# Kernel tuning notes

Measured on AMD Instinct MI355X. Metric: run time of the kernel, lower is better.

## Reference

```python
import jax, jax.numpy as jnp
import numpy as np

B, C, D, H, W = 1, 128, 8, 32, 32
NH, HD = 8, 16            # num_heads, head_dim = C // NH
PD, PH, PW = 2, 4, 4      # local patch dims
RD, RH, RW = 2, 2, 2      # global K/V reduction ratios
MLPH = 4 * C              # mlp_ratio = 4
EPS = 1e-5
SCALE = HD ** -0.5


def setup_inputs() -> dict:
    key = jax.random.key(0)
    ks = iter(jax.random.split(key, 16))
    def w(shape, scale=0.02):
        return jax.random.normal(next(ks), shape, jnp.float32) * scale
    inp = {"x": jax.random.normal(next(ks), (B, C, D, H, W), jnp.float32)}
    for p in ("l", "g"):  # local branch / global branch transformer blocks
        inp[f"{p}_n1_g"] = jnp.ones((C,), jnp.float32)
        inp[f"{p}_n1_b"] = jnp.zeros((C,), jnp.float32)
        inp[f"{p}_qkv_w"] = w((3 * C, C))            # Linear(dim, 3*dim, bias=False)
        inp[f"{p}_proj_w"] = w((C, C))
        inp[f"{p}_proj_b"] = jnp.zeros((C,), jnp.float32)
        inp[f"{p}_n2_g"] = jnp.ones((C,), jnp.float32)
        inp[f"{p}_n2_b"] = jnp.zeros((C,), jnp.float32)
        inp[f"{p}_fc1_w"] = w((MLPH, C))
        inp[f"{p}_fc1_b"] = jnp.zeros((MLPH,), jnp.float32)
        inp[f"{p}_fc2_w"] = w((C, MLPH))
        inp[f"{p}_fc2_b"] = jnp.zeros((C,), jnp.float32)
    inp["g_ke_w"] = w((C, C, RD, RH, RW))  # Conv3d(dim, dim, k=stride=(2,2,2), bias=False)
    inp["g_ve_w"] = w((C, C, RD, RH, RW))
    inp["g_nk_g"] = jnp.ones((HD,), jnp.float32)
    inp["g_nk_b"] = jnp.zeros((HD,), jnp.float32)
    inp["g_nv_g"] = jnp.ones((HD,), jnp.float32)
    inp["g_nv_b"] = jnp.zeros((HD,), jnp.float32)
    return inp


def _ln(t, g, b):
    m = t.mean(-1, keepdims=True)
    v = jnp.square(t - m).mean(-1, keepdims=True)
    return (t - m) * jax.lax.rsqrt(v + EPS) * g + b


def _mlp(t, w1, b1, w2, b2):
    return jax.nn.gelu(t @ w1.T + b1, approximate=False) @ w2.T + b2


def _forward(x, l_n1_g, l_n1_b, l_qkv_w, l_proj_w, l_proj_b, l_n2_g, l_n2_b,
             l_fc1_w, l_fc1_b, l_fc2_w, l_fc2_b,
             g_n1_g, g_n1_b, g_qkv_w, g_ke_w, g_ve_w, g_nk_g, g_nk_b,
             g_nv_g, g_nv_b, g_proj_w, g_proj_b, g_n2_g, g_n2_b,
             g_fc1_w, g_fc1_b, g_fc2_w, g_fc2_b):
    nd, nh, nw = D // PD, H // PH, W // PW
    R, Npl = nd * nh * nw, PD * PH * PW
    N = D * H * W

    # ---------------- Local branch ----------------
    # (B,C,D,H,W) -> (B, R, Npl, C) patch tokens
    loc = x.reshape(B, C, nd, PD, nh, PH, nw, PW)
    loc = loc.transpose(0, 2, 4, 6, 3, 5, 7, 1).reshape(B, R, Npl, C)
    y = _ln(loc, l_n1_g, l_n1_b)
    qkv = (y @ l_qkv_w.T).reshape(B, R, Npl, 3, NH, HD).transpose(3, 0, 1, 4, 2, 5)
    q, k, v = qkv[0], qkv[1], qkv[2]  # (B,R,NH,Npl,HD)
    attn = jax.nn.softmax(jnp.einsum('brhnd,brhmd->brhnm', q, k) * SCALE, axis=-1)
    o = jnp.einsum('brhnm,brhmd->brhnd', attn, v)
    # faithful to torch: (attn@v).transpose(-1,-2).reshape(B,R,Npl,C)
    o = jnp.swapaxes(o, -1, -2).reshape(B, R, Npl, C)
    loc = loc + (o @ l_proj_w.T + l_proj_b)
    loc = loc + _mlp(_ln(loc, l_n2_g, l_n2_b), l_fc1_w, l_fc1_b, l_fc2_w, l_fc2_b)
    # back to (B,C,D,H,W)
    loc_y = loc.reshape(B, nd, nh, nw, PD, PH, PW, C)
    loc_y = loc_y.transpose(0, 7, 1, 4, 2, 5, 3, 6).reshape(B, C, D, H, W)

    # ---------------- Global branch ----------------
    g = x.reshape(B, C, N).transpose(0, 2, 1)  # (B,N,C)
    y = _ln(g, g_n1_g, g_n1_b)
    qkv = y @ g_qkv_w.T  # (B,N,3C)
    q, k, v = jnp.split(qkv, 3, axis=-1)
    qh = q.reshape(B, N, NH, HD).transpose(0, 2, 1, 3)  # (B,NH,N,HD)
    dn = ('NCDHW', 'OIDHW', 'NCDHW')
    def _reduce(t, wc):
        tm = t.transpose(0, 2, 1).reshape(B, C, D, H, W)
        tr = jax.lax.conv_general_dilated(tm, wc, (RD, RH, RW), 'VALID',
                                          dimension_numbers=dn)
        nr = tr.shape[2] * tr.shape[3] * tr.shape[4]
        return tr.reshape(B, C, nr).transpose(0, 2, 1).reshape(B, nr, NH, HD).transpose(0, 2, 1, 3)
    kr = _ln(_reduce(k, g_ke_w), g_nk_g, g_nk_b)  # (B,NH,Nr,HD)
    vr = _ln(_reduce(v, g_ve_w), g_nv_g, g_nv_b)
    attn = jax.nn.softmax(jnp.einsum('bhnd,bhmd->bhnm', qh, kr) * SCALE, axis=-1)
    o = jnp.einsum('bhnm,bhmd->bhnd', attn, vr)
    o = o.transpose(0, 2, 1, 3).reshape(B, N, C)
    g = g + (o @ g_proj_w.T + g_proj_b)
    g = g + _mlp(_ln(g, g_n2_g, g_n2_b), g_fc1_w, g_fc1_b, g_fc2_w, g_fc2_b)
    glo_y = g.transpose(0, 2, 1).reshape(B, C, D, H, W)

    # ---------------- Gate ----------------
    return x * jax.nn.sigmoid(loc_y + glo_y)


def reference(x, l_n1_g, l_n1_b, l_qkv_w, l_proj_w, l_proj_b, l_n2_g, l_n2_b,
              l_fc1_w, l_fc1_b, l_fc2_w, l_fc2_b,
              g_n1_g, g_n1_b, g_qkv_w, g_ke_w, g_ve_w, g_nk_g, g_nk_b,
              g_nv_g, g_nv_b, g_proj_w, g_proj_b, g_n2_g, g_n2_b,
              g_fc1_w, g_fc1_b, g_fc2_w, g_fc2_b):
    return _forward(x, l_n1_g, l_n1_b, l_qkv_w, l_proj_w, l_proj_b, l_n2_g, l_n2_b,
                    l_fc1_w, l_fc1_b, l_fc2_w, l_fc2_b,
                    g_n1_g, g_n1_b, g_qkv_w, g_ke_w, g_ve_w, g_nk_g, g_nk_b,
                    g_nv_g, g_nv_b, g_proj_w, g_proj_b, g_n2_g, g_n2_b,
                    g_fc1_w, g_fc1_b, g_fc2_w, g_fc2_b)
```

## Files before the change

### kernel.cpp

```cpp
#include <hip/hip_runtime.h>
#include <math.h>

#define N_TOK 8192
#define C_DIM 128
#define NHD   8
#define HDIM  16
#define NR    1024
#define EPSV  1e-5f
#define QK_SCALE 0.25f

typedef __attribute__((ext_vector_type(8))) short short8;
typedef __attribute__((ext_vector_type(4))) float f32x4;

__device__ __forceinline__ float gelu_f(float v) {
    return 0.5f * v * (1.0f + erff(v * 0.70710678118654752f));
}
__device__ __forceinline__ float uaf(unsigned int u) {
    union { unsigned int u; float f; } x; x.u = u; return x.f;
}
__device__ __forceinline__ short f2b(float v) {
    union { float f; unsigned int u; } x; x.f = v;
    unsigned int r = x.u + 0x7fffu + ((x.u >> 16) & 1u);
    return (short)(r >> 16);
}
__device__ __forceinline__ void ld16bf(const short* p, float* d) {
    uint4 a = *(const uint4*)p;
    uint4 b = *(const uint4*)(p + 8);
    d[0]  = uaf(a.x << 16); d[1]  = uaf(a.x & 0xffff0000u);
    d[2]  = uaf(a.y << 16); d[3]  = uaf(a.y & 0xffff0000u);
    d[4]  = uaf(a.z << 16); d[5]  = uaf(a.z & 0xffff0000u);
    d[6]  = uaf(a.w << 16); d[7]  = uaf(a.w & 0xffff0000u);
    d[8]  = uaf(b.x << 16); d[9]  = uaf(b.x & 0xffff0000u);
    d[10] = uaf(b.y << 16); d[11] = uaf(b.y & 0xffff0000u);
    d[12] = uaf(b.z << 16); d[13] = uaf(b.z & 0xffff0000u);
    d[14] = uaf(b.w << 16); d[15] = uaf(b.w & 0xffff0000u);
}

struct CvtDesc { const float* src; short* dst; int n; int pad; };
struct CvtArgs { CvtDesc d[10]; };
__global__ __launch_bounds__(256) void cvtw_k(CvtArgs a) {
    CvtDesc dd = a.d[blockIdx.y];
    for (int i = blockIdx.x * 256 + threadIdx.x; i < dd.n; i += gridDim.x * 256)
        dd.dst[i] = f2b(dd.src[i]);
}

__global__ __launch_bounds__(256) void transpose_k(const float* __restrict__ x,
                                                   float* __restrict__ xt) {
    __shared__ float tile[32][33];
    int n0 = blockIdx.x * 32, c0 = blockIdx.y * 32;
    int tx = threadIdx.x, ty = threadIdx.y;
#pragma unroll
    for (int k = 0; k < 4; ++k)
        tile[ty + k * 8][tx] = x[(size_t)(c0 + ty + k * 8) * N_TOK + n0 + tx];
    __syncthreads();
#pragma unroll
    for (int k = 0; k < 4; ++k)
        xt[(size_t)(n0 + ty + k * 8) * C_DIM + c0 + tx] = tile[tx][ty + k * 8];
}

__global__ __launch_bounds__(256) void ln_token_k(const float* __restrict__ in,
                                                  const float* __restrict__ g1, const float* __restrict__ b1,
                                                  short* __restrict__ o1,
                                                  const float* __restrict__ g2, const float* __restrict__ b2,
                                                  short* __restrict__ o2) {
    int lane = threadIdx.x & 63;
    int n = blockIdx.x * 4 + (threadIdx.x >> 6);
    float v0 = in[(size_t)n * C_DIM + lane];
    float v1 = in[(size_t)n * C_DIM + 64 + lane];
    float s = v0 + v1, sq = v0 * v0 + v1 * v1;
#pragma unroll
    for (int off = 32; off >= 1; off >>= 1) {
        s += __shfl_xor(s, off);
        sq += __shfl_xor(sq, off);
    }
    float m = s * (1.0f / 128.0f);
    float var = sq * (1.0f / 128.0f) - m * m;
    float rs = rsqrtf(var + EPSV);
    float h0 = (v0 - m) * rs, h1 = (v1 - m) * rs;
    o1[(size_t)n * C_DIM + lane]      = f2b(h0 * g1[lane] + b1[lane]);
    o1[(size_t)n * C_DIM + 64 + lane] = f2b(h1 * g1[lane + 64] + b1[lane + 64]);
    o2[(size_t)n * C_DIM + lane]      = f2b(h0 * g2[lane] + b2[lane]);
    o2[(size_t)n * C_DIM + 64 + lane] = f2b(h1 * g2[lane + 64] + b2[lane + 64]);
}

__global__ __launch_bounds__(256) void ln2_pair_k(const float* __restrict__ in0,
                                                  const float* __restrict__ g0, const float* __restrict__ b0,
                                                  short* __restrict__ o0,
                                                  const float* __restrict__ in1,
                                                  const float* __restrict__ g1, const float* __restrict__ b1,
                                                  short* __restrict__ o1) {
    int blk = blockIdx.x;
    bool sel = blk >= 2048;
    blk &= 2047;
    const float* in = sel ? in1 : in0;
    const float* g  = sel ? g1 : g0;
    const float* b  = sel ? b1 : b0;
    short* o        = sel ? o1 : o0;
    int lane = threadIdx.x & 63;
    int n = blk * 4 + (threadIdx.x >> 6);
    float v0 = in[(size_t)n * C_DIM + lane];
    float v1 = in[(size_t)n * C_DIM + 64 + lane];
    float s = v0 + v1, sq = v0 * v0 + v1 * v1;
#pragma unroll
    for (int off = 32; off >= 1; off >>= 1) {
        s += __shfl_xor(s, off);
        sq += __shfl_xor(sq, off);
    }
    float m = s * (1.0f / 128.0f);
    float var = sq * (1.0f / 128.0f) - m * m;
    float rs = rsqrtf(var + EPSV);
    o[(size_t)n * C_DIM + lane]      = f2b((v0 - m) * rs * g[lane] + b[lane]);
    o[(size_t)n * C_DIM + 64 + lane] = f2b((v1 - m) * rs * g[lane + 64] + b[lane + 64]);
}

struct MArgs {
    const short* A[2]; const short* W[2];
    const float* bias[2]; const float* res[2];
    void* out[2];
};
template <int EPI>
__global__ __launch_bounds__(256) void mgemm_k(MArgs ga, int M, int N, int K, int kslice) {
    int zi    = (EPI == 3) ? (blockIdx.z >> 2) : blockIdx.z;
    int slice = (EPI == 3) ? (blockIdx.z & 3) : 0;
    const short* A = ga.A[zi];
    const short* W = ga.W[zi];
    __shared__ short As[128 * 64];
    __shared__ short Bs[128 * 64];
    int t = threadIdx.x;
    int w = t >> 6, l = t & 63;
    int m0 = blockIdx.x * 128, n0 = blockIdx.y * 128;
    int wm = (w >> 1) * 64, wn = (w & 1) * 64;
    int kbeg = (EPI == 3) ? slice * kslice : 0;
    int kend = kbeg + ((EPI == 3) ? kslice : K);

    f32x4 acc[4][4];
#pragma unroll
    for (int a = 0; a < 4; ++a)
#pragma unroll
        for (int b = 0; b < 4; ++b) acc[a][b] = f32x4{0.f, 0.f, 0.f, 0.f};

    for (int k0 = kbeg; k0 < kend; k0 += 64) {
        __syncthreads();
#pragma unroll
        for (int c = 0; c < 4; ++c) {
            int chunk = c * 256 + t;
            int row = chunk >> 3;
            int slot = chunk & 7;
            int ss = slot ^ (row & 7);
            uint4 av = *(const uint4*)(A + (size_t)(m0 + row) * K + k0 + slot * 8);
            *(uint4*)(As + row * 64 + ss * 8) = av;
            uint4 wv = *(const uint4*)(W + (size_t)(n0 + row) * K + k0 + slot * 8);
            *(uint4*)(Bs + row * 64 + ss * 8) = wv;
        }
        __syncthreads();
#pragma unroll
        for (int kk = 0; kk < 2; ++kk) {
            short8 af[4], bf[4];
            int sl = kk * 4 + (l >> 4);
#pragma unroll
            for (int mf = 0; mf < 4; ++mf) {
                int row = wm + mf * 16 + (l & 15);
                af[mf] = *(const short8*)(As + row * 64 + (sl ^ (row & 7)) * 8);
            }
#pragma unroll
            for (int nf = 0; nf < 4; ++nf) {
                int row = wn + nf * 16 + (l & 15);
                bf[nf] = *(const short8*)(Bs + row * 64 + (sl ^ (row & 7)) * 8);
            }
#pragma unroll
            for (int mf = 0; mf < 4; ++mf)
#pragma unroll
                for (int nf = 0; nf < 4; ++nf)
                    acc[mf][nf] = __builtin_amdgcn_mfma_f32_16x16x32_bf16(
                        af[mf], bf[nf], acc[mf][nf], 0, 0, 0);
        }
    }

#pragma unroll
    for (int mf = 0; mf < 4; ++mf) {
#pragma unroll
        for (int nf = 0; nf < 4; ++nf) {
            int col = n0 + wn + nf * 16 + (l & 15);
#pragma unroll
            for (int j = 0; j < 4; ++j) {
                int row = m0 + wm + mf * 16 + (l >> 4) * 4 + j;
                float v = acc[mf][nf][j];
                if (EPI == 0) {
                    ((short*)ga.out[zi])[(size_t)row * N + col] = f2b(v);
                } else if (EPI == 1) {
                    v += ga.bias[zi][col] + ga.res[zi][(size_t)row * N + col];
                    ((float*)ga.out[zi])[(size_t)row * N + col] = v;
                } else if (EPI == 2) {
                    v = gelu_f(v + ga.bias[zi][col]);
                    ((short*)ga.out[zi])[(size_t)row * N + col] = f2b(v);
                } else {
                    ((float*)ga.out[zi])[(size_t)slice * M * N + (size_t)row * N + col] = v;
                }
            }
        }
    }
}

__global__ __launch_bounds__(256) void local_attn_k(const short* __restrict__ qkv,
                                                    short* __restrict__ ob) {
    __shared__ float ks[NHD][32][HDIM];
    __shared__ float vs[NHD][32][HDIM];
    int m = threadIdx.x, h = threadIdx.y, r = blockIdx.x;
    int zd = r >> 6, zh = (r >> 3) & 7, zw = r & 7;
    int pd = m >> 4, ph = (m >> 2) & 3, pw = m & 3;
    int n = (zd * 2 + pd) * 1024 + (zh * 4 + ph) * 32 + (zw * 4 + pw);
    const short* base = qkv + (size_t)n * 384 + h * HDIM;
    float q[16], kt[16], vt[16];
    ld16bf(base, q);
    ld16bf(base + 128, kt);
    ld16bf(base + 256, vt);
#pragma unroll
    for (int d = 0; d < 16; ++d) { ks[h][m][d] = kt[d]; vs[h][m][d] = vt[d]; }
    __syncthreads();
    float s[32];
#pragma unroll
    for (int j = 0; j < 32; ++j) {
        float d = 0.f;
#pragma unroll
        for (int dd = 0; dd < 16; ++dd) d += q[dd] * ks[h][j][dd];
        s[j] = __expf(d * QK_SCALE);
    }
    float sum = 0.f;
#pragma unroll
    for (int j = 0; j < 32; ++j) sum += s[j];
    float inv = 1.0f / sum;
    float oo[16] = {};
#pragma unroll
    for (int j = 0; j < 32; ++j) {
        float p = s[j] * inv;
#pragma unroll
        for (int dd = 0; dd < 16; ++dd) oo[dd] += p * vs[h][j][dd];
    }
#pragma unroll
    for (int dd = 0; dd < 16; ++dd) {
        int n2 = h * 4 + (dd >> 2);
        int c2 = (dd & 3) * 32 + m;
        int pd2 = n2 >> 4, ph2 = (n2 >> 2) & 3, pw2 = n2 & 3;
        int nn = (zd * 2 + pd2) * 1024 + (zh * 4 + ph2) * 32 + (zw * 4 + pw2);
        ob[(size_t)nn * C_DIM + c2] = f2b(oo[dd]);
    }
}

__global__ __launch_bounds__(256) void gather_k(const short* __restrict__ qkv,
                                                short* __restrict__ kg, short* __restrict__ vg) {
    int idx = blockIdx.x * 256 + threadIdx.x;
    int nr = idx >> 10, qq = idx & 1023;
    int ci = qq >> 3, off = qq & 7;
    int od = off >> 2, oh = (off >> 1) & 1, ow = off & 1;
    int d2 = nr >> 8, h2 = (nr >> 4) & 15, w2 = nr & 15;
    int n = (2 * d2 + od) * 1024 + (2 * h2 + oh) * 32 + (2 * w2 + ow);
    kg[idx] = qkv[(size_t)n * 384 + 128 + ci];
    vg[idx] = qkv[(size_t)n * 384 + 256 + ci];
}

__global__ __launch_bounds__(256) void ln_head_sum_k(const float* __restrict__ kpart,
                                                     const float* __restrict__ vpart,
                                                     const float* __restrict__ gk, const float* __restrict__ bk,
                                                     const float* __restrict__ gv, const float* __restrict__ bv,
                                                     short* __restrict__ kout, short* __restrict__ vout) {
    int idx = blockIdx.x * 256 + threadIdx.x;
    bool sel = idx >= 8192;
    int id2 = idx & 8191;
    const float* part = sel ? vpart : kpart;
    const float* g    = sel ? gv : gk;
    const float* b    = sel ? bv : bk;
    int nr = id2 >> 3, h = id2 & 7;
    size_t base = (size_t)nr * C_DIM + h * HDIM;
    float v[16] = {};
#pragma unroll
    for (int p = 0; p < 4; ++p) {
        const float* pp = part + (size_t)p * (NR * C_DIM) + base;
#pragma unroll
        for (int d4 = 0; d4 < 4; ++d4) {
            float4 t = *(const float4*)(pp + d4 * 4);
            v[d4 * 4 + 0] += t.x; v[d4 * 4 + 1] += t.y;
            v[d4 * 4 + 2] += t.z; v[d4 * 4 + 3] += t.w;
        }
    }
    float s = 0.f;
#pragma unroll
    for (int i = 0; i < 16; ++i) s += v[i];
    float m = s * (1.0f / 16.0f);
    float sq = 0.f;
#pragma unroll
    for (int i = 0; i < 16; ++i) { float d = v[i] - m; sq += d * d; }
    float rs = rsqrtf(sq * (1.0f / 16.0f) + EPSV);
    if (!sel) {
        short* op = kout + (size_t)h * (NR * HDIM) + (size_t)nr * HDIM;
#pragma unroll
        for (int i = 0; i < 16; ++i)
            op[i] = f2b(((v[i] - m) * rs * g[i] + b[i]) * QK_SCALE);
    } else {
        short* op = vout + (size_t)h * (HDIM * NR) + nr;
#pragma unroll
        for (int i = 0; i < 16; ++i)
            op[(size_t)i * NR] = f2b((v[i] - m) * rs * g[i] + b[i]);
    }
}

__global__ __launch_bounds__(256) void gattn_k(const short* __restrict__ qkv,
                                               const short* __restrict__ kb,
                                               const short* __restrict__ vt,
                                               short* __restrict__ ob) {
    __shared__ short plds[4][2048];
    int t = threadIdx.x;
    int w = t >> 6, l = t & 63;
    int h = blockIdx.y;
    int lr = l & 15, lq = l >> 4;
    int q0 = blockIdx.x * 64 + w * 16;

    short8 qf = short8{0, 0, 0, 0, 0, 0, 0, 0};
    if (lq < 2)
        qf = *(const short8*)(qkv + (size_t)(q0 + lr) * 384 + h * HDIM + lq * 8);

    const short* kh = kb + (size_t)h * (NR * HDIM);
    const short* vh = vt + (size_t)h * (HDIM * NR);
    short* pw = &plds[w][0];

    const f32x4 zz = {0.f, 0.f, 0.f, 0.f};
    f32x4 oacc = {0.f, 0.f, 0.f, 0.f};
    float rs0 = 0.f, rs1 = 0.f, rs2 = 0.f, rs3 = 0.f;

    for (int c = 0; c < 8; ++c) {
        int kbase = c * 128;
        f32x4 s[8];
#pragma unroll
        for (int nf = 0; nf < 8; ++nf) {
            short8 kf = short8{0, 0, 0, 0, 0, 0, 0, 0};
            if (lq < 2)
                kf = *(const short8*)(kh + (size_t)(kbase + nf * 16 + lr) * HDIM + lq * 8);
            s[nf] = __builtin_amdgcn_mfma_f32_16x16x32_bf16(qf, kf, zz, 0, 0, 0);
        }
#pragma unroll
        for (int nf = 0; nf < 8; ++nf) {
            int key = nf * 16 + lr;
            float p0 = __expf(s[nf][0]);
            float p1 = __expf(s[nf][1]);
            float p2 = __expf(s[nf][2]);
            float p3 = __expf(s[nf][3]);
            rs0 += p0; rs1 += p1; rs2 += p2; rs3 += p3;
            int q_ = lq * 4;
            pw[((q_ + 0) * 128 + key) ^ (((q_ + 0) & 7) << 3)] = f2b(p0);
            pw[((q_ + 1) * 128 + key) ^ (((q_ + 1) & 7) << 3)] = f2b(p1);
            pw[((q_ + 2) * 128 + key) ^ (((q_ + 2) & 7) << 3)] = f2b(p2);
            pw[((q_ + 3) * 128 + key) ^ (((q_ + 3) & 7) << 3)] = f2b(p3);
        }
#pragma unroll
        for (int ks = 0; ks < 4; ++ks) {
            short8 pf = *(const short8*)&pw[(lr * 128 + ks * 32 + lq * 8) ^ ((lr & 7) << 3)];
            short8 vf = *(const short8*)(vh + (size_t)lr * NR + kbase + ks * 32 + lq * 8);
            oacc = __builtin_amdgcn_mfma_f32_16x16x32_bf16(pf, vf, oacc, 0, 0, 0);
        }
    }
#pragma unroll
    for (int off = 1; off <= 8; off <<= 1) {
        rs0 += __shfl_xor(rs0, off);
        rs1 += __shfl_xor(rs1, off);
        rs2 += __shfl_xor(rs2, off);
        rs3 += __shfl_xor(rs3, off);
    }
    size_t base_o = (size_t)(q0 + lq * 4) * C_DIM + h * HDIM + lr;
    ob[base_o]             = f2b(oacc[0] / rs0);
    ob[base_o + C_DIM]     = f2b(oacc[1] / rs1);
    ob[base_o + 2 * C_DIM] = f2b(oacc[2] / rs2);
    ob[base_o + 3 * C_DIM] = f2b(oacc[3] / rs3);
}

__global__ __launch_bounds__(256) void gate_k(const float* __restrict__ x,
                                              const float* __restrict__ lf, const float* __restrict__ gf,
                                              float* __restrict__ out) {
    __shared__ float tile[32][33];
    int n0 = blockIdx.x * 32, c0 = blockIdx.y * 32;
    int tx = threadIdx.x, ty = threadIdx.y;
#pragma unroll
    for (int k = 0; k < 4; ++k) {
        int n = n0 + ty + k * 8, c = c0 + tx;
        tile[ty + k * 8][tx] = lf[(size_t)n * C_DIM + c] + gf[(size_t)n * C_DIM + c];
    }
    __syncthreads();
#pragma unroll
    for (int k = 0; k < 4; ++k) {
        int c = c0 + ty + k * 8, n = n0 + tx;
        float z = tile[tx][ty + k * 8];
        float sg = 1.0f / (1.0f + __expf(-z));
        out[(size_t)c * N_TOK + n] = x[(size_t)c * N_TOK + n] * sg;
    }
}

extern "C" void kernel_launch(void* const* d_in, const int* in_sizes, int n_in,
                              void* d_out, int out_size, void* d_ws, size_t ws_size,
                              hipStream_t stream) {
    const float* x        = (const float*)d_in[0];
    const float* l_n1_g   = (const float*)d_in[1];
    const float* l_n1_b   = (const float*)d_in[2];
    const float* l_qkv_w  = (const float*)d_in[3];
    const float* l_proj_w = (const float*)d_in[4];
    const float* l_proj_b = (const float*)d_in[5];
    const float* l_n2_g   = (const float*)d_in[6];
    const float* l_n2_b   = (const float*)d_in[7];
    const float* l_fc1_w  = (const float*)d_in[8];
    const float* l_fc1_b  = (const float*)d_in[9];
    const float* l_fc2_w  = (const float*)d_in[10];
    const float* l_fc2_b  = (const float*)d_in[11];
    const float* g_n1_g   = (const float*)d_in[12];
    const float* g_n1_b   = (const float*)d_in[13];
    const float* g_qkv_w  = (const float*)d_in[14];
    const float* g_proj_w = (const float*)d_in[15];
    const float* g_proj_b = (const float*)d_in[16];
    const float* g_n2_g   = (const float*)d_in[17];
    const float* g_n2_b   = (const float*)d_in[18];
    const float* g_fc1_w  = (const float*)d_in[19];
    const float* g_fc1_b  = (const float*)d_in[20];
    const float* g_fc2_w  = (const float*)d_in[21];
    const float* g_fc2_b  = (const float*)d_in[22];
    const float* g_ke_w   = (const float*)d_in[23];
    const float* g_ve_w   = (const float*)d_in[24];
    const float* g_nk_g   = (const float*)d_in[25];
    const float* g_nk_b   = (const float*)d_in[26];
    const float* g_nv_g   = (const float*)d_in[27];
    const float* g_nv_b   = (const float*)d_in[28];
    float* out = (float*)d_out;

    char* base = (char*)d_ws;
    float* xt     = (float*)(base);
    float* t1_l   = (float*)(base + (4ull  << 20));
    float* t1_g   = (float*)(base + (8ull  << 20));
    short* yA16   = (short*)(base + (12ull << 20));
    short* yG16   = (short*)(base + (14ull << 20));
    short* t2_l   = yA16;
    short* t2_g   = yG16;
    float* locfin = (float*)(base + (12ull << 20));
    short* obuf_l = (short*)(base + (16ull << 20));
    short* obuf_g = (short*)(base + (18ull << 20));
    float* glofin = (float*)(base + (16ull << 20));
    short* qkv_l  = (short*)(base + (20ull << 20));
    short* qkv_g  = (short*)(base + (26ull << 20));
    short* h1_l   = (short*)(base + (32ull << 20));
    float* kpart  = (float*)(base + (32ull << 20));
    float* vpart  = (float*)(base + (34ull << 20));
    short* h1_g   = (short*)(base + (40ull << 20));
    short* kg16   = (short*)(base + (40ull << 20));
    short* vg16   = (short*)(base + (42ull << 20));
    short* kb16   = (short*)(base + (48ull << 20));
    short* vt16   = (short*)(base + (48ull << 20) + (512ull << 10));
    short* wts    = (short*)(base + (49ull << 20));

    const int L_QKV = 0,      L_PROJ = 49152, L_FC1 = 65536,  L_FC2 = 131072;
    const int G_QKV = 196608, G_PROJ = 245760, G_FC1 = 262144, G_FC2 = 327680;
    const int G_KE  = 393216, G_VE   = 524288;

    CvtArgs ca;
    ca.d[0] = {l_qkv_w,  wts + L_QKV,  49152, 0};
    ca.d[1] = {l_proj_w, wts + L_PROJ, 16384, 0};
    ca.d[2] = {l_fc1_w,  wts + L_FC1,  65536, 0};
    ca.d[3] = {l_fc2_w,  wts + L_FC2,  65536, 0};
    ca.d[4] = {g_qkv_w,  wts + G_QKV,  49152, 0};
    ca.d[5] = {g_proj_w, wts + G_PROJ, 16384, 0};
    ca.d[6] = {g_fc1_w,  wts + G_FC1,  65536, 0};
    ca.d[7] = {g_fc2_w,  wts + G_FC2,  65536, 0};
    ca.d[8] = {g_ke_w,   wts + G_KE,  131072, 0};
    ca.d[9] = {g_ve_w,   wts + G_VE,  131072, 0};

    cvtw_k<<<dim3(32, 10), 256, 0, stream>>>(ca);
    transpose_k<<<dim3(256, 4), dim3(32, 8), 0, stream>>>(x, xt);
    ln_token_k<<<2048, 256, 0, stream>>>(xt, l_n1_g, l_n1_b, yA16, g_n1_g, g_n1_b, yG16);

    MArgs a_qkv = {{yA16, yG16}, {wts + L_QKV, wts + G_QKV}, {nullptr, nullptr}, {nullptr, nullptr}, {qkv_l, qkv_g}};
    mgemm_k<0><<<dim3(64, 3, 2), 256, 0, stream>>>(a_qkv, N_TOK, 384, 128, 0);

    local_attn_k<<<256, dim3(32, 8), 0, stream>>>(qkv_l, obuf_l);
    gather_k<<<4096, 256, 0, stream>>>(qkv_g, kg16, vg16);

    MArgs a_cv = {{kg16, vg16}, {wts + G_KE, wts + G_VE}, {nullptr, nullptr}, {nullptr, nullptr}, {kpart, vpart}};
    mgemm_k<3><<<dim3(8, 1, 8), 256, 0, stream>>>(a_cv, NR, 128, 1024, 256);

    ln_head_sum_k<<<64, 256, 0, stream>>>(kpart, vpart, g_nk_g, g_nk_b, g_nv_g, g_nv_b, kb16, vt16);

    gattn_k<<<dim3(128, 8), 256, 0, stream>>>(qkv_g, kb16, vt16, obuf_g);

    MArgs a_pj = {{obuf_l, obuf_g}, {wts + L_PROJ, wts + G_PROJ}, {l_proj_b, g_proj_b}, {xt, xt}, {t1_l, t1_g}};
    mgemm_k<1><<<dim3(64, 1, 2), 256, 0, stream>>>(a_pj, N_TOK, 128, 128, 0);

    ln2_pair_k<<<4096, 256, 0, stream>>>(t1_l, l_n2_g, l_n2_b, t2_l, t1_g, g_n2_g, g_n2_b, t2_g);

    MArgs a_f1 = {{t2_l, t2_g}, {wts + L_FC1, wts + G_FC1}, {l_fc1_b, g_fc1_b}, {nullptr, nullptr}, {h1_l, h1_g}};
    mgemm_k<2><<<dim3(64, 4, 2), 256, 0, stream>>>(a_f1, N_TOK, 512, 128, 0);

    MArgs a_f2 = {{h1_l, h1_g}, {wts + L_FC2, wts + G_FC2}, {l_fc2_b, g_fc2_b}, {t1_l, t1_g}, {locfin, glofin}};
    mgemm_k<1><<<dim3(64, 1, 2), 256, 0, stream>>>(a_f2, N_TOK, 128, 512, 0);

    gate_k<<<dim3(256, 4), dim3(32, 8), 0, stream>>>(x, locfin, glofin, out);
}
```

Measured before the change: 143.8 us.

## Fuse prologue kernels, gather into local attn, gate into FC2 epilogue, tweak softmax

Merges weight conversion, input transpose and first LayerNorm into one kernel, and merges the K/V gather into the local attention launch. The sigmoid gate is fused into the global FC2 GEMM epilogue, which now reads the local result and x directly. The conv-reduction split-K is doubled to 8 slices. Global attention switches to exp2 with a folded log2e scale, a transposed score MFMA and packed bf16 conversion. These changes aim to cut launch count and intermediate round-trips, but the FC2 GEMMs are now serialized into two single-branch launches with half the blocks each.

New measurement: 156.9 us. +9.1%, slower.

```diff
diff --git a/kernel.cpp b/kernel.cpp
--- a/kernel.cpp
+++ b/kernel.cpp
@@ -8,6 +8,7 @@
 #define NR    1024
 #define EPSV  1e-5f
 #define QK_SCALE 0.25f
+#define QK_L2E  0.36067376f
 
 typedef __attribute__((ext_vector_type(8))) short short8;
 typedef __attribute__((ext_vector_type(4))) float f32x4;
@@ -38,49 +39,57 @@
 
 struct CvtDesc { const float* src; short* dst; int n; int pad; };
 struct CvtArgs { CvtDesc d[10]; };
-__global__ __launch_bounds__(256) void cvtw_k(CvtArgs a) {
-    CvtDesc dd = a.d[blockIdx.y];
-    for (int i = blockIdx.x * 256 + threadIdx.x; i < dd.n; i += gridDim.x * 256)
-        dd.dst[i] = f2b(dd.src[i]);
-}
-
-__global__ __launch_bounds__(256) void transpose_k(const float* __restrict__ x,
-                                                   float* __restrict__ xt) {
-    __shared__ float tile[32][33];
-    int n0 = blockIdx.x * 32, c0 = blockIdx.y * 32;
-    int tx = threadIdx.x, ty = threadIdx.y;
-#pragma unroll
-    for (int k = 0; k < 4; ++k)
-        tile[ty + k * 8][tx] = x[(size_t)(c0 + ty + k * 8) * N_TOK + n0 + tx];
+
+__global__ __launch_bounds__(256) void xlncvt_k(const float* __restrict__ x,
+                                                const float* __restrict__ g1, const float* __restrict__ b1,
+                                                const float* __restrict__ g2, const float* __restrict__ b2,
+                                                float* __restrict__ xt,
+                                                short* __restrict__ o1, short* __restrict__ o2,
+                                                CvtArgs ca) {
+    __shared__ float tile[64][130];
+    int t = threadIdx.x;
+    if (blockIdx.x >= 128) {
+        int bid = blockIdx.x - 128;
+#pragma unroll 1
+        for (int d = 0; d < 10; ++d) {
+            CvtDesc dd = ca.d[d];
+            for (int i = bid * 256 + t; i < dd.n; i += 40 * 256)
+                dd.dst[i] = f2b(dd.src[i]);
+        }
+        return;
+    }
+    int n0 = blockIdx.x * 64;
+#pragma unroll
+    for (int k = 0; k < 32; ++k) {
+        int flat = t + k * 256;
+        int n = flat & 63, c = flat >> 6;
+        tile[n][c] = x[(size_t)c * N_TOK + n0 + n];
+    }
     __syncthreads();
-#pragma unroll
-    for (int k = 0; k < 4; ++k)
-        xt[(size_t)(n0 + ty + k * 8) * C_DIM + c0 + tx] = tile[tx][ty + k * 8];
-}
-
-__global__ __launch_bounds__(256) void ln_token_k(const float* __restrict__ in,
-                                                  const float* __restrict__ g1, const float* __restrict__ b1,
-                                                  short* __restrict__ o1,
-                                                  const float* __restrict__ g2, const float* __restrict__ b2,
-                                                  short* __restrict__ o2) {
-    int lane = threadIdx.x & 63;
-    int n = blockIdx.x * 4 + (threadIdx.x >> 6);
-    float v0 = in[(size_t)n * C_DIM + lane];
-    float v1 = in[(size_t)n * C_DIM + 64 + lane];
-    float s = v0 + v1, sq = v0 * v0 + v1 * v1;
-#pragma unroll
-    for (int off = 32; off >= 1; off >>= 1) {
-        s += __shfl_xor(s, off);
-        sq += __shfl_xor(sq, off);
-    }
+    int tl = t >> 2, qt = t & 3;
+    float v[32];
+    float s = 0.f, sq = 0.f;
+#pragma unroll
+    for (int i = 0; i < 32; ++i) {
+        v[i] = tile[tl][qt * 32 + i];
+        s += v[i]; sq += v[i] * v[i];
+    }
+    s += __shfl_xor(s, 1);  s += __shfl_xor(s, 2);
+    sq += __shfl_xor(sq, 1); sq += __shfl_xor(sq, 2);
     float m = s * (1.0f / 128.0f);
     float var = sq * (1.0f / 128.0f) - m * m;
     float rs = rsqrtf(var + EPSV);
-    float h0 = (v0 - m) * rs, h1 = (v1 - m) * rs;
-    o1[(size_t)n * C_DIM + lane]      = f2b(h0 * g1[lane] + b1[lane]);
-    o1[(size_t)n * C_DIM + 64 + lane] = f2b(h1 * g1[lane + 64] + b1[lane + 64]);
-    o2[(size_t)n * C_DIM + lane]      = f2b(h0 * g2[lane] + b2[lane]);
-    o2[(size_t)n * C_DIM + 64 + lane] = f2b(h1 * g2[lane + 64] + b2[lane + 64]);
+    int tok = n0 + tl, cb = qt * 32;
+    float* xtp = xt + (size_t)tok * C_DIM + cb;
+    short* oA = o1 + (size_t)tok * C_DIM + cb;
+    short* oG = o2 + (size_t)tok * C_DIM + cb;
+#pragma unroll
+    for (int i = 0; i < 32; ++i) {
+        float hn = (v[i] - m) * rs;
+        xtp[i] = v[i];
+        oA[i] = f2b(hn * g1[cb + i] + b1[cb + i]);
+        oG[i] = f2b(hn * g2[cb + i] + b2[cb + i]);
+    }
 }
 
 __global__ __launch_bounds__(256) void ln2_pair_k(const float* __restrict__ in0,
@@ -117,11 +126,12 @@
     const short* A[2]; const short* W[2];
     const float* bias[2]; const float* res[2];
     void* out[2];
+    const float* aux0; const float* aux1;
 };
 template <int EPI>
 __global__ __launch_bounds__(256) void mgemm_k(MArgs ga, int M, int N, int K, int kslice) {
-    int zi    = (EPI == 3) ? (blockIdx.z >> 2) : blockIdx.z;
-    int slice = (EPI == 3) ? (blockIdx.z & 3) : 0;
+    int zi    = (EPI == 3) ? (blockIdx.z >> 3) : blockIdx.z;
+    int slice = (EPI == 3) ? (blockIdx.z & 7) : 0;
     const short* A = ga.A[zi];
     const short* W = ga.W[zi];
     __shared__ short As[128 * 64];
@@ -181,35 +191,64 @@
 #pragma unroll
         for (int nf = 0; nf < 4; ++nf) {
             int col = n0 + wn + nf * 16 + (l & 15);
-#pragma unroll
-            for (int j = 0; j < 4; ++j) {
-                int row = m0 + wm + mf * 16 + (l >> 4) * 4 + j;
-                float v = acc[mf][nf][j];
-                if (EPI == 0) {
-                    ((short*)ga.out[zi])[(size_t)row * N + col] = f2b(v);
-                } else if (EPI == 1) {
-                    v += ga.bias[zi][col] + ga.res[zi][(size_t)row * N + col];
-                    ((float*)ga.out[zi])[(size_t)row * N + col] = v;
-                } else if (EPI == 2) {
-                    v = gelu_f(v + ga.bias[zi][col]);
-                    ((short*)ga.out[zi])[(size_t)row * N + col] = f2b(v);
-                } else {
-                    ((float*)ga.out[zi])[(size_t)slice * M * N + (size_t)row * N + col] = v;
+            int rowb = m0 + wm + mf * 16 + (l >> 4) * 4;
+            if (EPI == 4) {
+                f32x4 xv = *(const f32x4*)(ga.aux1 + (size_t)col * N_TOK + rowb);
+                f32x4 ov;
+#pragma unroll
+                for (int j = 0; j < 4; ++j) {
+                    int row = rowb + j;
+                    float v = acc[mf][nf][j] + ga.bias[zi][col] + ga.res[zi][(size_t)row * N + col];
+                    float z = ga.aux0[(size_t)row * N + col] + v;
+                    float sg = 1.0f / (1.0f + __expf(-z));
+                    ov[j] = xv[j] * sg;
+                }
+                *(f32x4*)((float*)ga.out[zi] + (size_t)col * N_TOK + rowb) = ov;
+            } else {
+#pragma unroll
+                for (int j = 0; j < 4; ++j) {
+                    int row = rowb + j;
+                    float v = acc[mf][nf][j];
+                    if (EPI == 0) {
+                        ((short*)ga.out[zi])[(size_t)row * N + col] = f2b(v);
+                    } else if (EPI == 1) {
+                        v += ga.bias[zi][col] + ga.res[zi][(size_t)row * N + col];
+                        ((float*)ga.out[zi])[(size_t)row * N + col] = v;
+                    } else if (EPI == 2) {
+                        v = gelu_f(v + ga.bias[zi][col]);
+                        ((short*)ga.out[zi])[(size_t)row * N + col] = f2b(v);
+                    } else if (EPI == 3) {
+                        ((float*)ga.out[zi])[(size_t)slice * M * N + (size_t)row * N + col] = v;
+                    }
                 }
             }
         }
     }
 }
 
-__global__ __launch_bounds__(256) void local_attn_k(const short* __restrict__ qkv,
-                                                    short* __restrict__ ob) {
+__global__ __launch_bounds__(256) void lag_k(const short* __restrict__ qkv_l,
+                                             const short* __restrict__ qkv_g,
+                                             short* __restrict__ ob,
+                                             short* __restrict__ kg, short* __restrict__ vg) {
     __shared__ float ks[NHD][32][HDIM];
     __shared__ float vs[NHD][32][HDIM];
-    int m = threadIdx.x, h = threadIdx.y, r = blockIdx.x;
+    int t = threadIdx.x;
+    if (blockIdx.x >= 256) {
+        int idx = (blockIdx.x - 256) * 256 + t;
+        int nr = idx >> 10, qq = idx & 1023;
+        int ci = qq >> 3, off = qq & 7;
+        int od = off >> 2, oh = (off >> 1) & 1, ow = off & 1;
+        int d2 = nr >> 8, h2 = (nr >> 4) & 15, w2 = nr & 15;
+        int n = (2 * d2 + od) * 1024 + (2 * h2 + oh) * 32 + (2 * w2 + ow);
+        kg[idx] = qkv_g[(size_t)n * 384 + 128 + ci];
+        vg[idx] = qkv_g[(size_t)n * 384 + 256 + ci];
+        return;
+    }
+    int m = t & 31, h = t >> 5, r = blockIdx.x;
     int zd = r >> 6, zh = (r >> 3) & 7, zw = r & 7;
     int pd = m >> 4, ph = (m >> 2) & 3, pw = m & 3;
     int n = (zd * 2 + pd) * 1024 + (zh * 4 + ph) * 32 + (zw * 4 + pw);
-    const short* base = qkv + (size_t)n * 384 + h * HDIM;
+    const short* base = qkv_l + (size_t)n * 384 + h * HDIM;
     float q[16], kt[16], vt[16];
     ld16bf(base, q);
     ld16bf(base + 128, kt);
@@ -244,18 +283,6 @@
         int nn = (zd * 2 + pd2) * 1024 + (zh * 4 + ph2) * 32 + (zw * 4 + pw2);
         ob[(size_t)nn * C_DIM + c2] = f2b(oo[dd]);
     }
-}
-
-__global__ __launch_bounds__(256) void gather_k(const short* __restrict__ qkv,
-                                                short* __restrict__ kg, short* __restrict__ vg) {
-    int idx = blockIdx.x * 256 + threadIdx.x;
-    int nr = idx >> 10, qq = idx & 1023;
-    int ci = qq >> 3, off = qq & 7;
-    int od = off >> 2, oh = (off >> 1) & 1, ow = off & 1;
-    int d2 = nr >> 8, h2 = (nr >> 4) & 15, w2 = nr & 15;
-    int n = (2 * d2 + od) * 1024 + (2 * h2 + oh) * 32 + (2 * w2 + ow);
-    kg[idx] = qkv[(size_t)n * 384 + 128 + ci];
-    vg[idx] = qkv[(size_t)n * 384 + 256 + ci];
 }
 
 __global__ __launch_bounds__(256) void ln_head_sum_k(const float* __restrict__ kpart,
@@ -273,7 +300,7 @@
     size_t base = (size_t)nr * C_DIM + h * HDIM;
     float v[16] = {};
 #pragma unroll
-    for (int p = 0; p < 4; ++p) {
+    for (int p = 0; p < 8; ++p) {
         const float* pp = part + (size_t)p * (NR * C_DIM) + base;
 #pragma unroll
         for (int d4 = 0; d4 < 4; ++d4) {
@@ -294,7 +321,7 @@
         short* op = kout + (size_t)h * (NR * HDIM) + (size_t)nr * HDIM;
 #pragma unroll
         for (int i = 0; i < 16; ++i)
-            op[i] = f2b(((v[i] - m) * rs * g[i] + b[i]) * QK_SCALE);
+            op[i] = f2b(((v[i] - m) * rs * g[i] + b[i]) * QK_L2E);
     } else {
         short* op = vout + (size_t)h * (HDIM * NR) + nr;
 #pragma unroll
@@ -324,7 +351,7 @@
 
     const f32x4 zz = {0.f, 0.f, 0.f, 0.f};
     f32x4 oacc = {0.f, 0.f, 0.f, 0.f};
-    float rs0 = 0.f, rs1 = 0.f, rs2 = 0.f, rs3 = 0.f;
+    float rs = 0.f;
 
     for (int c = 0; c < 8; ++c) {
         int kbase = c * 128;
@@ -334,21 +361,22 @@
             short8 kf = short8{0, 0, 0, 0, 0, 0, 0, 0};
             if (lq < 2)
                 kf = *(const short8*)(kh + (size_t)(kbase + nf * 16 + lr) * HDIM + lq * 8);
-            s[nf] = __builtin_amdgcn_mfma_f32_16x16x32_bf16(qf, kf, zz, 0, 0, 0);
+            s[nf] = __builtin_amdgcn_mfma_f32_16x16x32_bf16(kf, qf, zz, 0, 0, 0);
         }
 #pragma unroll
         for (int nf = 0; nf < 8; ++nf) {
-            int key = nf * 16 + lr;
-            float p0 = __expf(s[nf][0]);
-            float p1 = __expf(s[nf][1]);
-            float p2 = __expf(s[nf][2]);
-            float p3 = __expf(s[nf][3]);
-            rs0 += p0; rs1 += p1; rs2 += p2; rs3 += p3;
-            int q_ = lq * 4;
-            pw[((q_ + 0) * 128 + key) ^ (((q_ + 0) & 7) << 3)] = f2b(p0);
-            pw[((q_ + 1) * 128 + key) ^ (((q_ + 1) & 7) << 3)] = f2b(p1);
-            pw[((q_ + 2) * 128 + key) ^ (((q_ + 2) & 7) << 3)] = f2b(p2);
-            pw[((q_ + 3) * 128 + key) ^ (((q_ + 3) & 7) << 3)] = f2b(p3);
+            float p0 = exp2f(s[nf][0]);
+            float p1 = exp2f(s[nf][1]);
+            float p2 = exp2f(s[nf][2]);
+            float p3 = exp2f(s[nf][3]);
+            rs += (p0 + p1) + (p2 + p3);
+            unsigned int u01, u23;
+            asm("v_cvt_pk_bf16_f32 %0, %1, %2" : "=v"(u01) : "v"(p0), "v"(p1));
+            asm("v_cvt_pk_bf16_f32 %0, %1, %2" : "=v"(u23) : "v"(p2), "v"(p3));
+            int k0 = nf * 16 + lq * 4;
+            int sw = (lr & 7) << 3;
+            *(unsigned int*)&pw[lr * 128 + (k0 ^ sw)]       = u01;
+            *(unsigned int*)&pw[lr * 128 + ((k0 + 2) ^ sw)] = u23;
         }
 #pragma unroll
         for (int ks = 0; ks < 4; ++ks) {
@@ -357,39 +385,17 @@
             oacc = __builtin_amdgcn_mfma_f32_16x16x32_bf16(pf, vf, oacc, 0, 0, 0);
         }
     }
-#pragma unroll
-    for (int off = 1; off <= 8; off <<= 1) {
-        rs0 += __shfl_xor(rs0, off);
-        rs1 += __shfl_xor(rs1, off);
-        rs2 += __shfl_xor(rs2, off);
-        rs3 += __shfl_xor(rs3, off);
-    }
+    rs += __shfl_xor(rs, 16);
+    rs += __shfl_xor(rs, 32);
+    float r0 = __shfl(rs, lq * 4 + 0);
+    float r1 = __shfl(rs, lq * 4 + 1);
+    float r2 = __shfl(rs, lq * 4 + 2);
+    float r3 = __shfl(rs, lq * 4 + 3);
     size_t base_o = (size_t)(q0 + lq * 4) * C_DIM + h * HDIM + lr;
-    ob[base_o]             = f2b(oacc[0] / rs0);
-    ob[base_o + C_DIM]     = f2b(oacc[1] / rs1);
-    ob[base_o + 2 * C_DIM] = f2b(oacc[2] / rs2);
-    ob[base_o + 3 * C_DIM] = f2b(oacc[3] / rs3);
-}
-
-__global__ __launch_bounds__(256) void gate_k(const float* __restrict__ x,
-                                              const float* __restrict__ lf, const float* __restrict__ gf,
-                                              float* __restrict__ out) {
-    __shared__ float tile[32][33];
-    int n0 = blockIdx.x * 32, c0 = blockIdx.y * 32;
-    int tx = threadIdx.x, ty = threadIdx.y;
-#pragma unroll
-    for (int k = 0; k < 4; ++k) {
-        int n = n0 + ty + k * 8, c = c0 + tx;
-        tile[ty + k * 8][tx] = lf[(size_t)n * C_DIM + c] + gf[(size_t)n * C_DIM + c];
-    }
-    __syncthreads();
-#pragma unroll
-    for (int k = 0; k < 4; ++k) {
-        int c = c0 + ty + k * 8, n = n0 + tx;
-        float z = tile[tx][ty + k * 8];
-        float sg = 1.0f / (1.0f + __expf(-z));
-        out[(size_t)c * N_TOK + n] = x[(size_t)c * N_TOK + n] * sg;
-    }
+    ob[base_o]             = f2b(oacc[0] / r0);
+    ob[base_o + C_DIM]     = f2b(oacc[1] / r1);
+    ob[base_o + 2 * C_DIM] = f2b(oacc[2] / r2);
+    ob[base_o + 3 * C_DIM] = f2b(oacc[3] / r3);
 }
 
 extern "C" void kernel_launch(void* const* d_in, const int* in_sizes, int n_in,
@@ -437,12 +443,11 @@
     float* locfin = (float*)(base + (12ull << 20));
     short* obuf_l = (short*)(base + (16ull << 20));
     short* obuf_g = (short*)(base + (18ull << 20));
-    float* glofin = (float*)(base + (16ull << 20));
     short* qkv_l  = (short*)(base + (20ull << 20));
     short* qkv_g  = (short*)(base + (26ull << 20));
     short* h1_l   = (short*)(base + (32ull << 20));
     float* kpart  = (float*)(base + (32ull << 20));
-    float* vpart  = (float*)(base + (34ull << 20));
+    float* vpart  = (float*)(base + (36ull << 20));
     short* h1_g   = (short*)(base + (40ull << 20));
     short* kg16   = (short*)(base + (40ull << 20));
     short* vg16   = (short*)(base + (42ull << 20));
@@ -466,33 +471,31 @@
     ca.d[8] = {g_ke_w,   wts + G_KE,  131072, 0};
     ca.d[9] = {g_ve_w,   wts + G_VE,  131072, 0};
 
-    cvtw_k<<<dim3(32, 10), 256, 0, stream>>>(ca);
-    transpose_k<<<dim3(256, 4), dim3(32, 8), 0, stream>>>(x, xt);
-    ln_token_k<<<2048, 256, 0, stream>>>(xt, l_n1_g, l_n1_b, yA16, g_n1_g, g_n1_b, yG16);
-
-    MArgs a_qkv = {{yA16, yG16}, {wts + L_QKV, wts + G_QKV}, {nullptr, nullptr}, {nullptr, nullptr}, {qkv_l, qkv_g}};
+    xlncvt_k<<<168, 256, 0, stream>>>(x, l_n1_g, l_n1_b, g_n1_g, g_n1_b, xt, yA16, yG16, ca);
+
+    MArgs a_qkv = {{yA16, yG16}, {wts + L_QKV, wts + G_QKV}, {nullptr, nullptr}, {nullptr, nullptr}, {qkv_l, qkv_g}, nullptr, nullptr};
     mgemm_k<0><<<dim3(64, 3, 2), 256, 0, stream>>>(a_qkv, N_TOK, 384, 128, 0);
 
-    local_attn_k<<<256, dim3(32, 8), 0, stream>>>(qkv_l, obuf_l);
-    gather_k<<<4096, 256, 0, stream>>>(qkv_g, kg16, vg16);
-
-    MArgs a_cv = {{kg16, vg16}, {wts + G_KE, wts + G_VE}, {nullptr, nullptr}, {nullptr, nullptr}, {kpart, vpart}};
-    mgemm_k<3><<<dim3(8, 1, 8), 256, 0, stream>>>(a_cv, NR, 128, 1024, 256);
+    lag_k<<<4352, 256, 0, stream>>>(qkv_l, qkv_g, obuf_l, kg16, vg16);
+
+    MArgs a_cv = {{kg16, vg16}, {wts + G_KE, wts + G_VE}, {nullptr, nullptr}, {nullptr, nullptr}, {kpart, vpart}, nullptr, nullptr};
+    mgemm_k<3><<<dim3(8, 1, 16), 256, 0, stream>>>(a_cv, NR, 128, 1024, 128);
 
     ln_head_sum_k<<<64, 256, 0, stream>>>(kpart, vpart, g_nk_g, g_nk_b, g_nv_g, g_nv_b, kb16, vt16);
 
     gattn_k<<<dim3(128, 8), 256, 0, stream>>>(qkv_g, kb16, vt16, obuf_g);
 
-    MArgs a_pj = {{obuf_l, obuf_g}, {wts + L_PROJ, wts + G_PROJ}, {l_proj_b, g_proj_b}, {xt, xt}, {t1_l, t1_g}};
+    MArgs a_pj = {{obuf_l, obuf_g}, {wts + L_PROJ, wts + G_PROJ}, {l_proj_b, g_proj_b}, {xt, xt}, {t1_l, t1_g}, nullptr, nullptr};
     mgemm_k<1><<<dim3(64, 1, 2), 256, 0, stream>>>(a_pj, N_TOK, 128, 128, 0);
 
     ln2_pair_k<<<4096, 256, 0, stream>>>(t1_l, l_n2_g, l_n2_b, t2_l, t1_g, g_n2_g, g_n2_b, t2_g);
 
-    MArgs a_f1 = {{t2_l, t2_g}, {wts + L_FC1, wts + G_FC1}, {l_fc1_b, g_fc1_b}, {nullptr, nullptr}, {h1_l, h1_g}};
+    MArgs a_f1 = {{t2_l, t2_g}, {wts + L_FC1, wts + G_FC1}, {l_fc1_b, g_fc1_b}, {nullptr, nullptr}, {h1_l, h1_g}, nullptr, nullptr};
     mgemm_k<2><<<dim3(64, 4, 2), 256, 0, stream>>>(a_f1, N_TOK, 512, 128, 0);
 
-    MArgs a_f2 = {{h1_l, h1_g}, {wts + L_FC2, wts + G_FC2}, {l_fc2_b, g_fc2_b}, {t1_l, t1_g}, {locfin, glofin}};
-    mgemm_k<1><<<dim3(64, 1, 2), 256, 0, stream>>>(a_f2, N_TOK, 128, 512, 0);
-
-    gate_k<<<dim3(256, 4), dim3(32, 8), 0, stream>>>(x, locfin, glofin, out);
-}
+    MArgs a_f2l = {{h1_l, nullptr}, {wts + L_FC2, nullptr}, {l_fc2_b, nullptr}, {t1_l, nullptr}, {locfin, nullptr}, nullptr, nullptr};
+    mgemm_k<1><<<dim3(64, 1, 1), 256, 0, stream>>>(a_f2l, N_TOK, 128, 512, 0);
+
+    MArgs a_f2g = {{h1_g, nullptr}, {wts + G_FC2, nullptr}, {g_fc2_b, nullptr}, {t1_g, nullptr}, {out, nullptr}, locfin, x};
+    mgemm_k<4><<<dim3(64, 1, 1), 256, 0, stream>>>(a_f2g, N_TOK, 128, 512, 0);
+}
```
